# Performance work log

Measured on AMD Instinct MI355X. Metric: run time of the kernel, lower is better.

Reference implementation:

```python
import jax, jax.numpy as jnp
import numpy as np

B, L, H, HS, OUT = 4, 512, 768, 64, 16  # batch, seq_len, hidden, head_size, output_size


def setup_inputs() -> dict:
    key = jax.random.key(0)
    ks = jax.random.split(key, 4)
    return {
        "x": jax.random.normal(ks[0], (B, L, H), dtype=jnp.float32),
        "Wq": jax.random.normal(ks[1], (H, HS), dtype=jnp.float32) * 0.02,
        "bq": jnp.zeros((HS,), dtype=jnp.float32),
        "Wk": jax.random.normal(ks[2], (H, HS), dtype=jnp.float32) * 0.02,
        "bk": jnp.zeros((HS,), dtype=jnp.float32),
        "Wb": jax.random.normal(ks[3], (4 * HS, OUT), dtype=jnp.float32) * 0.02,
        "bb": jnp.zeros((OUT,), dtype=jnp.float32),
    }


def _tri_indices(seq_len):
    # pair p corresponds to (start=i, end=j) with j >= i, ordered by i then j
    idx_start = np.repeat(np.arange(seq_len), np.arange(seq_len, 0, -1))
    idx_end = np.concatenate([np.arange(i, seq_len) for i in range(seq_len)])
    return idx_start, idx_end


def reference(x, Wq, bq, Wk, bk, Wb, bb):
    seq_len = x.shape[1]
    idx_start, idx_end = _tri_indices(seq_len)  # static numpy, P = L*(L+1)/2

    # Project per-token first (math-equivalent to projecting the gathered
    # pair tensors, since Linear is applied token-wise), then gather pairs.
    q = x @ Wq + bq  # [B, L, HS]
    k = x @ Wk + bk  # [B, L, HS]

    q_start = q[:, idx_start]  # query(start_token_hidden)  [B, P, HS]
    q_end = q[:, idx_end]      # query(end_token_hidden)
    k_end = k[:, idx_end]      # key(end_token_hidden) == key_start == key_end

    # entity_type_bias(cat([query_start, key_start, query_end, key_end]))
    feat = jnp.concatenate([q_start, k_end, q_end, k_end], axis=-1) @ Wb + bb  # [B, P, OUT]

    # einsum('blnh,blnh->bln') with n=1 -> per-pair dot product, broadcast over OUT
    score = jnp.einsum('bph,bph->bp', q_start, k_end)[..., None]  # [B, P, 1]
    return score + feat  # [B, P, OUT]
```

## Files before the change

### kernel.cpp

```cpp
#include <hip/hip_runtime.h>
#include <hip/hip_bf16.h>

#define Bc   4
#define Lc   512
#define Hc   768
#define HSc  64
#define OUTc 16
#define Pc   131328
#define KH   384


__global__ __launch_bounds__(256) void qk_proj_kernel(
    const float* __restrict__ x,
    const float* __restrict__ Wq, const float* __restrict__ bq,
    const float* __restrict__ Wk, const float* __restrict__ bk,
    const float* __restrict__ Wb, const float* __restrict__ bb,
    float* __restrict__ qws, float* __restrict__ kws,
    float* __restrict__ Aws, float* __restrict__ Ews)
{
    __shared__ float lds_p[2][4][128];
    __shared__ float lds_c[4][128];

    const int tid = threadIdx.x;
    const int n   = tid & 127;
    const int wu  = __builtin_amdgcn_readfirstlane(tid >> 6);
    const int kh  = wu >> 1;
    const bool is_q = ((wu & 1) == 0);
    const int col = n & 63;
    const int tok_base = blockIdx.x * 4;

    const float* Wp = is_q ? Wq : Wk;
    const float* wp = Wp + (size_t)kh * KH * HSc + col;
    const float* xr = x + (size_t)tok_base * Hc + kh * KH;

    float acc0 = 0.f, acc1 = 0.f, acc2 = 0.f, acc3 = 0.f;
    for (int j0 = 0; j0 < KH; j0 += 16) {
        float w[16];
        #pragma unroll
        for (int u = 0; u < 16; ++u)
            w[u] = wp[(j0 + u) * HSc];
        #pragma unroll
        for (int u = 0; u < 16; ++u) {
            const int jj = j0 + u;
            const float x0 = xr[jj];
            const float x1 = xr[Hc + jj];
            const float x2 = xr[2 * Hc + jj];
            const float x3 = xr[3 * Hc + jj];
            acc0 += x0 * w[u];
            acc1 += x1 * w[u];
            acc2 += x2 * w[u];
            acc3 += x3 * w[u];
        }
    }

    lds_p[kh][0][n] = acc0;
    lds_p[kh][1][n] = acc1;
    lds_p[kh][2][n] = acc2;
    lds_p[kh][3][n] = acc3;
    __syncthreads();

    for (int i = tid; i < 512; i += 256) {
        const int t = i >> 7;
        const int c = i & 127;
        float v = lds_p[0][t][c] + lds_p[1][t][c];
        const int cc = c & 63;
        if (c < 64) { v += bq[cc]; qws[(size_t)(tok_base + t) * HSc + cc] = v; }
        else        { v += bk[cc]; kws[(size_t)(tok_base + t) * HSc + cc] = v; }
        lds_c[t][c] = v;
    }
    __syncthreads();

    if (tid < 128) {
        const int t = tid >> 5;
        const int c = tid & 31;
        const int tok = tok_base + t;
        const float* row = lds_c[t];
        if (c < 16) {
            float a = 0.f;
            #pragma unroll 8
            for (int h = 0; h < 64; ++h)
                a += row[h] * Wb[h * OUTc + c];
            Aws[(size_t)tok * OUTc + c] = a;
        } else {
            const int o = c - 16;
            float ev = bb[o];
            #pragma unroll 8
            for (int h = 0; h < 64; ++h) {
                ev += row[h]      * Wb[(128 + h) * OUTc + o];
                ev += row[64 + h] * (Wb[(64 + h) * OUTc + o] + Wb[(192 + h) * OUTc + o]);
            }
            Ews[(size_t)tok * OUTc + o] = ev;
        }
    }
}

__global__ __launch_bounds__(256) void pair_kernel(
    const float* __restrict__ qws, const float* __restrict__ kws,
    const float* __restrict__ Aws, const float* __restrict__ Ews,
    float* __restrict__ out)
{
    __shared__ alignas(16) float lds_q[2][HSc];
    __shared__ alignas(16) float lds_A[2][OUTc];

    const int j = blockIdx.x;
    const int b = blockIdx.y;
    const int s1 = j;
    const int s2 = Lc - 1 - j;
    const int n1 = Lc - s1;

    const int tid = threadIdx.x;
    if (tid < 64) {
        lds_q[0][tid] = qws[((size_t)b * Lc + s1) * HSc + tid];
    } else if (tid < 128) {
        lds_q[1][tid - 64] = qws[((size_t)b * Lc + s2) * HSc + (tid - 64)];
    } else if (tid < 144) {
        lds_A[0][tid - 128] = Aws[((size_t)b * Lc + s1) * OUTc + (tid - 128)];
    } else if (tid < 160) {
        lds_A[1][tid - 144] = Aws[((size_t)b * Lc + s2) * OUTc + (tid - 144)];
    }
    __syncthreads();

    const int P1 = s1 * (2 * Lc + 1 - s1) / 2;
    const int P2 = s2 * (2 * Lc + 1 - s2) / 2;
    const int lane = tid & 3;

    const float* kb = kws + (size_t)b * Lc * HSc;
    const float* Eb = Ews + (size_t)b * Lc * OUTc;
    float* ob = out + (size_t)b * Pc * OUTc;

    for (int p = tid >> 2; p < Lc + 1; p += 64) {
        const int which = (p < n1) ? 0 : 1;
        const int e   = which ? (s2 + (p - n1)) : (s1 + p);
        const int row = which ? (P2 + (p - n1)) : (P1 + p);

        const float4* kk = (const float4*)(kb + (size_t)e * HSc);
        const float4* qq = (const float4*)lds_q[which];

        float sc = 0.f;
        #pragma unroll
        for (int i = 0; i < 4; ++i) {
            float4 kv = kk[i * 4 + lane];
            float4 qv = qq[i * 4 + lane];
            sc += qv.x * kv.x + qv.y * kv.y + qv.z * kv.z + qv.w * kv.w;
        }
        sc += __shfl_xor(sc, 1);
        sc += __shfl_xor(sc, 2);

        const float4 ev = ((const float4*)(Eb + (size_t)e * OUTc))[lane];
        const float4 av = ((const float4*)lds_A[which])[lane];
        float4 r;
        r.x = av.x + ev.x + sc;
        r.y = av.y + ev.y + sc;
        r.z = av.z + ev.z + sc;
        r.w = av.w + ev.w + sc;
        ((float4*)(ob + (size_t)row * OUTc))[lane] = r;
    }
}

extern "C" void kernel_launch(void* const* d_in, const int* in_sizes, int n_in,
                              void* d_out, int out_size, void* d_ws, size_t ws_size,
                              hipStream_t stream) {
    const float* x  = (const float*)d_in[0];
    const float* Wq = (const float*)d_in[1];
    const float* bq = (const float*)d_in[2];
    const float* Wk = (const float*)d_in[3];
    const float* bk = (const float*)d_in[4];
    const float* Wb = (const float*)d_in[5];
    const float* bb = (const float*)d_in[6];

    float* ws  = (float*)d_ws;
    float* qws = ws;
    float* kws = ws + 131072;
    float* Aws = ws + 262144;
    float* Ews = ws + 294912;

    qk_proj_kernel<<<dim3(512), dim3(256), 0, stream>>>(
        x, Wq, bq, Wk, bk, Wb, bb, qws, kws, Aws, Ews);
    pair_kernel<<<dim3(256, 4), dim3(256), 0, stream>>>(
        qws, kws, Aws, Ews, (float*)d_out);
}
```

Measured before the change: 108.5 us.

## Split projection K-dimension four ways, double-buffer weights, unroll pair loop with nontemporal stores

The projection kernel now runs 512 threads per block and splits the 768-long reduction into four 192-wide segments, so more waves share the work, with a four-way LDS reduction at the end. Weight loads are double-buffered so the next 16 rows are fetched while the current ones are multiplied. In the pair kernel the strided loop is fully unrolled, key and E loads are issued before the arithmetic, and output goes through nontemporal stores to avoid polluting cache. A dummy read of Ews multiplied by zero is added, apparently to shape scheduling, at the cost of an extra load.

```diff
diff --git a/kernel.cpp b/kernel.cpp
--- a/kernel.cpp
+++ b/kernel.cpp
@@ -7,10 +7,12 @@
 #define HSc  64
 #define OUTc 16
 #define Pc   131328
-#define KH   384
-
-
-__global__ __launch_bounds__(256) void qk_proj_kernel(
+#define KSEG 192
+
+typedef float floatx4 __attribute__((ext_vector_type(4)));
+
+
+__global__ __launch_bounds__(512, 4) void qk_proj_kernel(
     const float* __restrict__ x,
     const float* __restrict__ Wq, const float* __restrict__ bq,
     const float* __restrict__ Wk, const float* __restrict__ bk,
@@ -18,27 +20,30 @@
     float* __restrict__ qws, float* __restrict__ kws,
     float* __restrict__ Aws, float* __restrict__ Ews)
 {
-    __shared__ float lds_p[2][4][128];
+    __shared__ float lds_p[4][4][128];
     __shared__ float lds_c[4][128];
 
     const int tid = threadIdx.x;
-    const int n   = tid & 127;
     const int wu  = __builtin_amdgcn_readfirstlane(tid >> 6);
-    const int kh  = wu >> 1;
-    const bool is_q = ((wu & 1) == 0);
-    const int col = n & 63;
+    const int half = wu & 1;
+    const int kseg = wu >> 1;
+    const int col  = tid & 63;
     const int tok_base = blockIdx.x * 4;
 
-    const float* Wp = is_q ? Wq : Wk;
-    const float* wp = Wp + (size_t)kh * KH * HSc + col;
-    const float* xr = x + (size_t)tok_base * Hc + kh * KH;
+    const float* Wp = half ? Wk : Wq;
+    const float* wp = Wp + (size_t)kseg * KSEG * HSc + col;
+    const float* xr = x + (size_t)tok_base * Hc + kseg * KSEG;
 
     float acc0 = 0.f, acc1 = 0.f, acc2 = 0.f, acc3 = 0.f;
-    for (int j0 = 0; j0 < KH; j0 += 16) {
-        float w[16];
+    float wA[16], wB[16];
+
+    #pragma unroll
+    for (int u = 0; u < 16; ++u) wA[u] = wp[u * HSc];
+
+    #pragma unroll 1
+    for (int j0 = 0; j0 < KSEG; j0 += 32) {
         #pragma unroll
-        for (int u = 0; u < 16; ++u)
-            w[u] = wp[(j0 + u) * HSc];
+        for (int u = 0; u < 16; ++u) wB[u] = wp[(j0 + 16 + u) * HSc];
         #pragma unroll
         for (int u = 0; u < 16; ++u) {
             const int jj = j0 + u;
@@ -46,23 +51,40 @@
             const float x1 = xr[Hc + jj];
             const float x2 = xr[2 * Hc + jj];
             const float x3 = xr[3 * Hc + jj];
-            acc0 += x0 * w[u];
-            acc1 += x1 * w[u];
-            acc2 += x2 * w[u];
-            acc3 += x3 * w[u];
-        }
-    }
-
-    lds_p[kh][0][n] = acc0;
-    lds_p[kh][1][n] = acc1;
-    lds_p[kh][2][n] = acc2;
-    lds_p[kh][3][n] = acc3;
+            acc0 += x0 * wA[u];
+            acc1 += x1 * wA[u];
+            acc2 += x2 * wA[u];
+            acc3 += x3 * wA[u];
+        }
+        if (j0 + 32 < KSEG) {
+            #pragma unroll
+            for (int u = 0; u < 16; ++u) wA[u] = wp[(j0 + 32 + u) * HSc];
+        }
+        #pragma unroll
+        for (int u = 0; u < 16; ++u) {
+            const int jj = j0 + 16 + u;
+            const float x0 = xr[jj];
+            const float x1 = xr[Hc + jj];
+            const float x2 = xr[2 * Hc + jj];
+            const float x3 = xr[3 * Hc + jj];
+            acc0 += x0 * wB[u];
+            acc1 += x1 * wB[u];
+            acc2 += x2 * wB[u];
+            acc3 += x3 * wB[u];
+        }
+    }
+
+    const int n = half * 64 + col;
+    lds_p[kseg][0][n] = acc0;
+    lds_p[kseg][1][n] = acc1;
+    lds_p[kseg][2][n] = acc2;
+    lds_p[kseg][3][n] = acc3;
     __syncthreads();
 
-    for (int i = tid; i < 512; i += 256) {
-        const int t = i >> 7;
-        const int c = i & 127;
-        float v = lds_p[0][t][c] + lds_p[1][t][c];
+    if (tid < 512) {
+        const int t = tid >> 7;
+        const int c = tid & 127;
+        float v = lds_p[0][t][c] + lds_p[1][t][c] + lds_p[2][t][c] + lds_p[3][t][c];
         const int cc = c & 63;
         if (c < 64) { v += bq[cc]; qws[(size_t)(tok_base + t) * HSc + cc] = v; }
         else        { v += bk[cc]; kws[(size_t)(tok_base + t) * HSc + cc] = v; }
@@ -116,19 +138,20 @@
     } else if (tid < 144) {
         lds_A[0][tid - 128] = Aws[((size_t)b * Lc + s1) * OUTc + (tid - 128)];
     } else if (tid < 160) {
-        lds_A[1][tid - 144] = Aws[((size_t)b * Lc + s2) * OUTc + (tid - 144)];
+        lds_A[1][tid - 144] = Ews[0] * 0.f + Aws[((size_t)b * Lc + s2) * OUTc + (tid - 144)];
     }
     __syncthreads();
 
     const int P1 = s1 * (2 * Lc + 1 - s1) / 2;
     const int P2 = s2 * (2 * Lc + 1 - s2) / 2;
     const int lane = tid & 3;
+    const int slot = tid >> 2;
 
     const float* kb = kws + (size_t)b * Lc * HSc;
     const float* Eb = Ews + (size_t)b * Lc * OUTc;
     float* ob = out + (size_t)b * Pc * OUTc;
 
-    for (int p = tid >> 2; p < Lc + 1; p += 64) {
+    auto do_pair = [&](int p) {
         const int which = (p < n1) ? 0 : 1;
         const int e   = which ? (s2 + (p - n1)) : (s1 + p);
         const int row = which ? (P2 + (p - n1)) : (P1 + p);
@@ -136,25 +159,39 @@
         const float4* kk = (const float4*)(kb + (size_t)e * HSc);
         const float4* qq = (const float4*)lds_q[which];
 
-        float sc = 0.f;
-        #pragma unroll
-        for (int i = 0; i < 4; ++i) {
-            float4 kv = kk[i * 4 + lane];
-            float4 qv = qq[i * 4 + lane];
-            sc += qv.x * kv.x + qv.y * kv.y + qv.z * kv.z + qv.w * kv.w;
-        }
+        float4 kv0 = kk[lane];
+        float4 kv1 = kk[4 + lane];
+        float4 kv2 = kk[8 + lane];
+        float4 kv3 = kk[12 + lane];
+        const float4 ev = ((const float4*)(Eb + (size_t)e * OUTc))[lane];
+
+        float4 qv0 = qq[lane];
+        float4 qv1 = qq[4 + lane];
+        float4 qv2 = qq[8 + lane];
+        float4 qv3 = qq[12 + lane];
+
+        float sc = qv0.x * kv0.x + qv0.y * kv0.y + qv0.z * kv0.z + qv0.w * kv0.w;
+        sc += qv1.x * kv1.x + qv1.y * kv1.y + qv1.z * kv1.z + qv1.w * kv1.w;
+        sc += qv2.x * kv2.x + qv2.y * kv2.y + qv2.z * kv2.z + qv2.w * kv2.w;
+        sc += qv3.x * kv3.x + qv3.y * kv3.y + qv3.z * kv3.z + qv3.w * kv3.w;
         sc += __shfl_xor(sc, 1);
         sc += __shfl_xor(sc, 2);
 
-        const float4 ev = ((const float4*)(Eb + (size_t)e * OUTc))[lane];
         const float4 av = ((const float4*)lds_A[which])[lane];
-        float4 r;
+        floatx4 r;
         r.x = av.x + ev.x + sc;
         r.y = av.y + ev.y + sc;
         r.z = av.z + ev.z + sc;
         r.w = av.w + ev.w + sc;
-        ((float4*)(ob + (size_t)row * OUTc))[lane] = r;
-    }
+        __builtin_nontemporal_store(r, (floatx4*)(ob + (size_t)row * OUTc) + lane);
+    };
+
+    #pragma unroll
+    for (int i = 0; i < 4; ++i) {
+        do_pair(slot + 128 * i);
+        do_pair(slot + 128 * i + 64);
+    }
+    if (slot == 0) do_pair(512);
 }
 
 extern "C" void kernel_launch(void* const* d_in, const int* in_sizes, int n_in,
@@ -174,7 +211,7 @@
     float* Aws = ws + 262144;
     float* Ews = ws + 294912;
 
-    qk_proj_kernel<<<dim3(512), dim3(256), 0, stream>>>(
+    qk_proj_kernel<<<dim3(512), dim3(512), 0, stream>>>(
         x, Wq, bq, Wk, bk, Wb, bb, qws, kws, Aws, Ews);
     pair_kernel<<<dim3(256, 4), dim3(256), 0, stream>>>(
         qws, kws, Aws, Ews, (float*)d_out);
```

New measurement: 100.2 us. 7.7% less time.
